# Performance work log

Hardware: AMD Instinct MI355X
Metric: run time of the kernel (lower is better)

## Reference

```python
import jax, jax.numpy as jnp
import numpy as np

B, D = 8192, 256
NUM_CLASSES = 128
CHUNK = 256          # matches module chunk_size; B % CHUNK == 0
TEMP = 0.07
EPS_NORM = 1e-12


def setup_inputs() -> dict:
    key = jax.random.key(0)
    k1, k2 = jax.random.split(key)
    features = jax.random.normal(k1, (B, D), dtype=jnp.float32)
    labels = jax.random.randint(k2, (B,), 0, NUM_CLASSES, dtype=jnp.int64)
    return {"features": features, "labels": labels}


def reference(features, labels):
    n = features.shape[0]
    temperature = max(TEMP, 1e-4)

    # F.normalize(dim=1): x / max(||x||, eps)
    norm = jnp.maximum(jnp.linalg.norm(features, axis=1, keepdims=True), EPS_NORM)
    f = features / norm
    # clamp is a no-op after normalization but kept for faithfulness
    f = jnp.clip(f, -1000.0, 1000.0)

    # [B, B] similarity; the torch loop computes exactly these rows chunk by chunk
    sim = jnp.matmul(f, f.T) / temperature

    # self-mask: each row i masks column i (diagonal of its chunk's square block)
    self_mask = ~jnp.eye(n, dtype=bool)

    # positive mask: same label, excluding self
    pos = (labels[:, None] == labels[None, :]) & self_mask
    # per-chunk fallback: if a 256-row chunk has no positives at all, use self_mask
    pos_c = pos.reshape(n // CHUNK, CHUNK, n)
    has_pos = pos_c.any(axis=(1, 2), keepdims=True)
    pos = jnp.where(has_pos, pos_c, self_mask.reshape(n // CHUNK, CHUNK, n)).reshape(n, n)

    # max-subtract BEFORE self-masking (faithful: includes self-sim = 1/temp)
    sim_max = jnp.max(sim, axis=1, keepdims=True)
    logits = jnp.clip(sim - jax.lax.stop_gradient(sim_max), -1000.0, 1000.0)

    exp_sim = jnp.maximum(jnp.exp(logits), 1e-8) * self_mask
    log_sum_exp = jnp.log(jnp.sum(exp_sim, axis=1, keepdims=True) + 1e-8)
    log_prob = jnp.maximum(logits - log_sum_exp, -1000.0)

    pos_pairs = jnp.sum(pos, axis=1)                      # [B] int
    row_loss = -jnp.sum(pos * log_prob, axis=1)           # [B]
    valid = pos_pairs > 0
    row_loss = jnp.where(valid, row_loss / jnp.maximum(pos_pairs, 1).astype(row_loss.dtype), 0.0)

    total_loss = jnp.sum(row_loss)
    total_pairs = jnp.sum(valid).astype(jnp.float32)
    mean_loss = total_loss / (total_pairs + 1e-8)
    loss = mean_loss  # reduction == 'mean'
    return loss, total_pairs, mean_loss
```

## Files before the change

### kernel.cpp

```cpp
#include <hip/hip_runtime.h>
#include <hip/hip_bf16.h>
#include <type_traits>

#define NB 8192
#define DD 256
#define INV_T (1.0f/0.07f)
#define LOG2E 1.4426950408889634f
#define LN2   0.6931471805599453f
#define K1    (INV_T*LOG2E)
#define NSPLIT 8
#define BM 128
#define BN 64
#define CPS (NB/NSPLIT)
#define NITER (CPS/BN)
#define BUFB (BN*DD*2)

typedef __attribute__((ext_vector_type(8))) short s8v;
typedef __attribute__((ext_vector_type(4))) float f4v;
typedef unsigned int u32;
typedef unsigned short u16;

#define OFF_FB   0
#define OFF_SE   (4*1024*1024)
#define OFF_SP   (OFF_SE + NSPLIT*NB*4)
#define OFF_CL   (OFF_SP + NSPLIT*NB*4)
#define OFF_CV   (OFF_CL + 256)
#define OFF_CNT  (OFF_CV + 256)

__global__ void k_norm(const float* __restrict__ feat,
                       __hip_bfloat16* __restrict__ fb, int* __restrict__ cnt) {
    if (blockIdx.x == 0 && threadIdx.x == 0) *cnt = 0;
    const int t = threadIdx.x;
    const int w = t >> 6, l = t & 63;
    const int row = blockIdx.x * 4 + w;
    const float4 v = ((const float4*)feat)[row * 64 + l];
    float s = v.x * v.x + v.y * v.y + v.z * v.z + v.w * v.w;
    #pragma unroll
    for (int d = 32; d; d >>= 1) s += __shfl_xor(s, d, 64);
    const float scale = 1.0f / fmaxf(sqrtf(s), 1e-12f);
    __hip_bfloat16 h0 = __float2bfloat16(v.x * scale);
    __hip_bfloat16 h1 = __float2bfloat16(v.y * scale);
    __hip_bfloat16 h2 = __float2bfloat16(v.z * scale);
    __hip_bfloat16 h3 = __float2bfloat16(v.w * scale);
    ushort4 o;
    o.x = *(u16*)&h0; o.y = *(u16*)&h1; o.z = *(u16*)&h2; o.w = *(u16*)&h3;
    ((ushort4*)fb)[row * 64 + l] = o;
}

__launch_bounds__(256, 2)
__global__ void k_main(const __hip_bfloat16* __restrict__ fb,
                       const int* __restrict__ lab,
                       float* __restrict__ SE, float* __restrict__ SP) {
    __shared__ __align__(16) char ldsB[2 * BUFB];
    __shared__ int ldsLab[CPS];
    const int tid = threadIdx.x;
    const int l = tid & 63;
    const int l15 = l & 15, lg = l >> 4;
    const int bid = blockIdx.x;
    const int sp = bid & 7, rb = bid >> 3;
    const int wbase = rb * BM + (tid >> 6) * 32;
    const int col0 = sp * CPS;

    #pragma unroll
    for (int i = 0; i < 4; i++)
        ldsLab[tid + i * 256] = lab[col0 + tid + i * 256];

    s8v a[2][8];
    #pragma unroll
    for (int m = 0; m < 2; m++)
        #pragma unroll
        for (int kk = 0; kk < 8; kk++)
            a[m][kk] = *(const s8v*)(fb + (wbase + m * 16 + l15) * DD + kk * 32 + lg * 8);

    int labr[8];
    #pragma unroll
    for (int m = 0; m < 2; m++)
        #pragma unroll
        for (int r = 0; r < 4; r++)
            labr[m * 4 + r] = lab[wbase + m * 16 + lg * 4 + r];

    float sE[8], sPp[8];
    #pragma unroll
    for (int i = 0; i < 8; i++) { sE[i] = 0.f; sPp[i] = 0.f; }

    s8v st[8];
    auto load_tile = [&](int t) {
        const char* gsrc = (const char*)fb + (size_t)(col0 + t * BN) * (DD * 2);
        #pragma unroll
        for (int i = 0; i < 8; i++)
            st[i] = *(const s8v*)(gsrc + tid * 16 + i * 4096);
    };
    auto write_tile = [&](int bufoff) {
        #pragma unroll
        for (int i = 0; i < 8; i++) {
            const int x = tid * 16 + i * 4096;
            const int br = x >> 9, inrow = x & 511;
            *(s8v*)(ldsB + bufoff + (br * 512 | (inrow ^ ((br & 7) << 4)))) = st[i];
        }
    };

    auto run = [&](auto diagC) {
        constexpr bool DIAG = decltype(diagC)::value;
        load_tile(0);
        write_tile(0);
        __syncthreads();
        for (int t = 0; t < NITER; t++) {
            const int curoff = (t & 1) * BUFB;
            if (t + 1 < NITER) load_tile(t + 1);

            f4v acc[2][4];
            #pragma unroll
            for (int m = 0; m < 2; m++)
                #pragma unroll
                for (int n = 0; n < 4; n++)
                    acc[m][n] = (f4v){0.f, 0.f, 0.f, 0.f};

            #pragma unroll
            for (int kk = 0; kk < 8; kk++) {
                s8v bfr[4];
                #pragma unroll
                for (int n = 0; n < 4; n++) {
                    const int br = n * 16 + l15;
                    const int ad = (br * 512 + kk * 64 + lg * 16) ^ ((br & 7) << 4);
                    bfr[n] = *(const s8v*)(ldsB + curoff + ad);
                }
                #pragma unroll
                for (int m = 0; m < 2; m++)
                    #pragma unroll
                    for (int n = 0; n < 4; n++)
                        acc[m][n] = __builtin_amdgcn_mfma_f32_16x16x32_bf16(a[m][kk], bfr[n], acc[m][n], 0, 0, 0);
            }

            const int cb = col0 + t * BN;
            #pragma unroll
            for (int n = 0; n < 4; n++) {
                const int col = cb + n * 16 + l15;
                const int lc = ldsLab[t * BN + n * 16 + l15];
                #pragma unroll
                for (int m = 0; m < 2; m++)
                    #pragma unroll
                    for (int r = 0; r < 4; r++) {
                        const int idx = m * 4 + r;
                        const float lg2 = fmaf(acc[m][n][r], K1, -K1);
                        float e = fmaxf(exp2f(lg2), 1e-8f);
                        bool pos = (lc == labr[idx]);
                        if (DIAG) {
                            const int row = wbase + m * 16 + lg * 4 + r;
                            const bool nself = (row != col);
                            e = nself ? e : 0.f;
                            pos = pos && nself;
                        }
                        sE[idx] += e;
                        sPp[idx] += pos ? lg2 : 0.f;
                    }
            }

            if (t + 1 < NITER) write_tile(curoff ^ BUFB);
            __syncthreads();
        }
    };
    if ((rb >> 3) == sp) run(std::true_type{}); else run(std::false_type{});

    #pragma unroll
    for (int idx = 0; idx < 8; idx++) {
        #pragma unroll
        for (int d = 1; d < 16; d <<= 1) {
            sE[idx]  += __shfl_xor(sE[idx], d, 16);
            sPp[idx] += __shfl_xor(sPp[idx], d, 16);
        }
    }
    if (l15 == 0) {
        #pragma unroll
        for (int idx = 0; idx < 8; idx++) {
            const int row = wbase + (idx >> 2) * 16 + lg * 4 + (idx & 3);
            SE[sp * NB + row] = sE[idx];
            SP[sp * NB + row] = sPp[idx];
        }
    }
}

__global__ void k_rows(const int* __restrict__ lab,
                       const float* __restrict__ SE, const float* __restrict__ SP,
                       float* __restrict__ CL, float* __restrict__ CV,
                       int* __restrict__ cnt, float* __restrict__ out) {
    __shared__ int h[128];
    const int t = threadIdx.x;
    if (t < 128) h[t] = 0;
    __syncthreads();
    #pragma unroll
    for (int i = 0; i < 32; i++)
        atomicAdd(&h[lab[t + i * 256]], 1);
    __syncthreads();

    const int row = blockIdx.x * 256 + t;
    float se = 0.f, sp_ = 0.f;
    #pragma unroll
    for (int s = 0; s < NSPLIT; s++) {
        se  += SE[s * NB + row];
        sp_ += SP[s * NB + row];
    }
    const int n = h[lab[row]] - 1;
    const float lse = logf(se + 1e-8f);
    const bool valid = n > 0;
    float loss = valid ? (lse - sp_ * LN2 / (float)n) : 0.f;
    float vf = valid ? 1.f : 0.f;
    #pragma unroll
    for (int d = 32; d; d >>= 1) { loss += __shfl_xor(loss, d, 64); vf += __shfl_xor(vf, d, 64); }
    __shared__ float pl[4], pv[4];
    __shared__ int isLast;
    if ((t & 63) == 0) { pl[t >> 6] = loss; pv[t >> 6] = vf; }
    __syncthreads();
    if (t == 0) {
        CL[blockIdx.x] = pl[0] + pl[1] + pl[2] + pl[3];
        CV[blockIdx.x] = pv[0] + pv[1] + pv[2] + pv[3];
        __threadfence();
        isLast = (atomicAdd(cnt, 1) == 31);
    }
    __syncthreads();
    if (isLast) {
        __threadfence();
        float lsum = (t < 32) ? CL[t] : 0.f;
        float vsum = (t < 32) ? CV[t] : 0.f;
        #pragma unroll
        for (int d = 32; d; d >>= 1) { lsum += __shfl_xor(lsum, d, 64); vsum += __shfl_xor(vsum, d, 64); }
        if (t == 0) {
            const float mean = lsum / (vsum + 1e-8f);
            out[0] = mean;
            out[1] = vsum;
            out[2] = mean;
        }
    }
}

extern "C" void kernel_launch(void* const* d_in, const int* in_sizes, int n_in,
                              void* d_out, int out_size, void* d_ws, size_t ws_size,
                              hipStream_t stream) {
    (void)in_sizes; (void)n_in; (void)out_size; (void)ws_size;
    const float* feat = (const float*)d_in[0];
    const int*   lab  = (const int*)d_in[1];
    char* ws = (char*)d_ws;
    __hip_bfloat16* fb = (__hip_bfloat16*)(ws + OFF_FB);
    float* SE = (float*)(ws + OFF_SE);
    float* SP = (float*)(ws + OFF_SP);
    float* CL = (float*)(ws + OFF_CL);
    float* CV = (float*)(ws + OFF_CV);
    int*   cnt = (int*)(ws + OFF_CNT);
    float* out = (float*)d_out;

    hipLaunchKernelGGL(k_norm, dim3(NB / 4), dim3(256), 0, stream, feat, fb, cnt);
    hipLaunchKernelGGL(k_main, dim3(NB / BM * NSPLIT), dim3(256), 0, stream, fb, lab, SE, SP);
    hipLaunchKernelGGL(k_rows, dim3(NB / 256), dim3(256), 0, stream, lab, SE, SP, CL, CV, cnt, out);
}
```

Baseline: 71.67 us.

## Use 512-thread blocks and fold temperature offset into the final reduction

Row-block size doubles to 256 with 512-thread workgroups, so each LDS column tile is shared by 8 waves and each thread loads half as much of it. The epilogue drops the per-element fma and the 1e-8 clamp: it exponentiates sim*K1 directly and sums raw dot products for positives. The constant max offset (exp(-1/T) and n/T) is applied once per row in k_rows. Dropping the clamp slightly changes semantics for tiny exponentials, and the larger block may reduce occupancy and block-level scheduling flexibility.

```diff
diff --git a/kernel.cpp b/kernel.cpp
--- a/kernel.cpp
+++ b/kernel.cpp
@@ -6,10 +6,10 @@
 #define DD 256
 #define INV_T (1.0f/0.07f)
 #define LOG2E 1.4426950408889634f
-#define LN2   0.6931471805599453f
 #define K1    (INV_T*LOG2E)
+#define CEXP  6.2087204553847255e-7f
 #define NSPLIT 8
-#define BM 128
+#define BM 256
 #define BN 64
 #define CPS (NB/NSPLIT)
 #define NITER (CPS/BN)
@@ -47,7 +47,7 @@
     ((ushort4*)fb)[row * 64 + l] = o;
 }
 
-__launch_bounds__(256, 2)
+__launch_bounds__(512)
 __global__ void k_main(const __hip_bfloat16* __restrict__ fb,
                        const int* __restrict__ lab,
                        float* __restrict__ SE, float* __restrict__ SP) {
@@ -61,9 +61,8 @@
     const int wbase = rb * BM + (tid >> 6) * 32;
     const int col0 = sp * CPS;
 
-    #pragma unroll
-    for (int i = 0; i < 4; i++)
-        ldsLab[tid + i * 256] = lab[col0 + tid + i * 256];
+    ldsLab[tid]       = lab[col0 + tid];
+    ldsLab[tid + 512] = lab[col0 + 512 + tid];
 
     s8v a[2][8];
     #pragma unroll
@@ -79,21 +78,21 @@
         for (int r = 0; r < 4; r++)
             labr[m * 4 + r] = lab[wbase + m * 16 + lg * 4 + r];
 
-    float sE[8], sPp[8];
-    #pragma unroll
-    for (int i = 0; i < 8; i++) { sE[i] = 0.f; sPp[i] = 0.f; }
-
-    s8v st[8];
+    float sE[8], sPa[8];
+    #pragma unroll
+    for (int i = 0; i < 8; i++) { sE[i] = 0.f; sPa[i] = 0.f; }
+
+    s8v st[4];
     auto load_tile = [&](int t) {
         const char* gsrc = (const char*)fb + (size_t)(col0 + t * BN) * (DD * 2);
         #pragma unroll
-        for (int i = 0; i < 8; i++)
-            st[i] = *(const s8v*)(gsrc + tid * 16 + i * 4096);
+        for (int i = 0; i < 4; i++)
+            st[i] = *(const s8v*)(gsrc + tid * 16 + i * 8192);
     };
     auto write_tile = [&](int bufoff) {
         #pragma unroll
-        for (int i = 0; i < 8; i++) {
-            const int x = tid * 16 + i * 4096;
+        for (int i = 0; i < 4; i++) {
+            const int x = tid * 16 + i * 8192;
             const int br = x >> 9, inrow = x & 511;
             *(s8v*)(ldsB + bufoff + (br * 512 | (inrow ^ ((br & 7) << 4)))) = st[i];
         }
@@ -108,6 +107,11 @@
             const int curoff = (t & 1) * BUFB;
             if (t + 1 < NITER) load_tile(t + 1);
 
+            int lc[4];
+            #pragma unroll
+            for (int n = 0; n < 4; n++)
+                lc[n] = ldsLab[t * BN + n * 16 + l15];
+
             f4v acc[2][4];
             #pragma unroll
             for (int m = 0; m < 2; m++)
@@ -117,56 +121,67 @@
 
             #pragma unroll
             for (int kk = 0; kk < 8; kk++) {
-                s8v bfr[4];
-                #pragma unroll
-                for (int n = 0; n < 4; n++) {
-                    const int br = n * 16 + l15;
-                    const int ad = (br * 512 + kk * 64 + lg * 16) ^ ((br & 7) << 4);
-                    bfr[n] = *(const s8v*)(ldsB + curoff + ad);
+                s8v b0, b1;
+                {
+                    const int br0 = 0 * 16 + l15, br1 = 1 * 16 + l15;
+                    b0 = *(const s8v*)(ldsB + curoff + ((br0 * 512 + kk * 64 + lg * 16) ^ ((br0 & 7) << 4)));
+                    b1 = *(const s8v*)(ldsB + curoff + ((br1 * 512 + kk * 64 + lg * 16) ^ ((br1 & 7) << 4)));
                 }
-                #pragma unroll
-                for (int m = 0; m < 2; m++)
-                    #pragma unroll
-                    for (int n = 0; n < 4; n++)
-                        acc[m][n] = __builtin_amdgcn_mfma_f32_16x16x32_bf16(a[m][kk], bfr[n], acc[m][n], 0, 0, 0);
+                acc[0][0] = __builtin_amdgcn_mfma_f32_16x16x32_bf16(a[0][kk], b0, acc[0][0], 0, 0, 0);
+                acc[1][0] = __builtin_amdgcn_mfma_f32_16x16x32_bf16(a[1][kk], b0, acc[1][0], 0, 0, 0);
+                acc[0][1] = __builtin_amdgcn_mfma_f32_16x16x32_bf16(a[0][kk], b1, acc[0][1], 0, 0, 0);
+                acc[1][1] = __builtin_amdgcn_mfma_f32_16x16x32_bf16(a[1][kk], b1, acc[1][1], 0, 0, 0);
             }
+            #pragma unroll
+            for (int kk = 0; kk < 8; kk++) {
+                s8v b2, b3;
+                {
+                    const int br2 = 2 * 16 + l15, br3 = 3 * 16 + l15;
+                    b2 = *(const s8v*)(ldsB + curoff + ((br2 * 512 + kk * 64 + lg * 16) ^ ((br2 & 7) << 4)));
+                    b3 = *(const s8v*)(ldsB + curoff + ((br3 * 512 + kk * 64 + lg * 16) ^ ((br3 & 7) << 4)));
+                }
+                acc[0][2] = __builtin_amdgcn_mfma_f32_16x16x32_bf16(a[0][kk], b2, acc[0][2], 0, 0, 0);
+                acc[1][2] = __builtin_amdgcn_mfma_f32_16x16x32_bf16(a[1][kk], b2, acc[1][2], 0, 0, 0);
+                acc[0][3] = __builtin_amdgcn_mfma_f32_16x16x32_bf16(a[0][kk], b3, acc[0][3], 0, 0, 0);
+                acc[1][3] = __builtin_amdgcn_mfma_f32_16x16x32_bf16(a[1][kk], b3, acc[1][3], 0, 0, 0);
+            }
 
             const int cb = col0 + t * BN;
-            #pragma unroll
-            for (int n = 0; n < 4; n++) {
-                const int col = cb + n * 16 + l15;
-                const int lc = ldsLab[t * BN + n * 16 + l15];
+            auto ep = [&](int n) {
                 #pragma unroll
                 for (int m = 0; m < 2; m++)
                     #pragma unroll
                     for (int r = 0; r < 4; r++) {
                         const int idx = m * 4 + r;
-                        const float lg2 = fmaf(acc[m][n][r], K1, -K1);
-                        float e = fmaxf(exp2f(lg2), 1e-8f);
-                        bool pos = (lc == labr[idx]);
+                        const float v = acc[m][n][r];
+                        float e = exp2f(v * K1);
+                        bool pos = (lc[n] == labr[idx]);
                         if (DIAG) {
                             const int row = wbase + m * 16 + lg * 4 + r;
+                            const int col = cb + n * 16 + l15;
                             const bool nself = (row != col);
                             e = nself ? e : 0.f;
                             pos = pos && nself;
                         }
                         sE[idx] += e;
-                        sPp[idx] += pos ? lg2 : 0.f;
+                        sPa[idx] += pos ? v : 0.f;
                     }
-            }
+            };
+            ep(0); ep(1);
+            ep(2); ep(3);
 
             if (t + 1 < NITER) write_tile(curoff ^ BUFB);
             __syncthreads();
         }
     };
-    if ((rb >> 3) == sp) run(std::true_type{}); else run(std::false_type{});
+    if ((rb >> 2) == sp) run(std::true_type{}); else run(std::false_type{});
 
     #pragma unroll
     for (int idx = 0; idx < 8; idx++) {
         #pragma unroll
         for (int d = 1; d < 16; d <<= 1) {
             sE[idx]  += __shfl_xor(sE[idx], d, 16);
-            sPp[idx] += __shfl_xor(sPp[idx], d, 16);
+            sPa[idx] += __shfl_xor(sPa[idx], d, 16);
         }
     }
     if (l15 == 0) {
@@ -174,7 +189,7 @@
         for (int idx = 0; idx < 8; idx++) {
             const int row = wbase + (idx >> 2) * 16 + lg * 4 + (idx & 3);
             SE[sp * NB + row] = sE[idx];
-            SP[sp * NB + row] = sPp[idx];
+            SP[sp * NB + row] = sPa[idx];
         }
     }
 }
@@ -193,16 +208,16 @@
     __syncthreads();
 
     const int row = blockIdx.x * 256 + t;
-    float se = 0.f, sp_ = 0.f;
+    float se = 0.f, spa = 0.f;
     #pragma unroll
     for (int s = 0; s < NSPLIT; s++) {
         se  += SE[s * NB + row];
-        sp_ += SP[s * NB + row];
+        spa += SP[s * NB + row];
     }
     const int n = h[lab[row]] - 1;
-    const float lse = logf(se + 1e-8f);
+    const float lse = logf(se * CEXP + 1e-8f);
     const bool valid = n > 0;
-    float loss = valid ? (lse - sp_ * LN2 / (float)n) : 0.f;
+    float loss = valid ? (lse - (spa - (float)n) * INV_T / (float)n) : 0.f;
     float vf = valid ? 1.f : 0.f;
     #pragma unroll
     for (int d = 32; d; d >>= 1) { loss += __shfl_xor(loss, d, 64); vf += __shfl_xor(vf, d, 64); }
@@ -248,6 +263,6 @@
     float* out = (float*)d_out;
 
     hipLaunchKernelGGL(k_norm, dim3(NB / 4), dim3(256), 0, stream, feat, fb, cnt);
-    hipLaunchKernelGGL(k_main, dim3(NB / BM * NSPLIT), dim3(256), 0, stream, fb, lab, SE, SP);
+    hipLaunchKernelGGL(k_main, dim3(NB / BM * NSPLIT), dim3(512), 0, stream, fb, lab, SE, SP);
     hipLaunchKernelGGL(k_rows, dim3(NB / 256), dim3(256), 0, stream, lab, SE, SP, CL, CV, cnt, out);
 }
```

Result: no change. 70.73 us (-1.3%).

## Exploit similarity symmetry: compute upper-triangle tiles and emit row and column partial sums

Applied to the files above, without the earlier changes.

The main kernel now iterates only over upper-triangular 256x256 tiles (528 blocks of 512 threads), using the symmetry of f·fᵀ. Each off-diagonal tile accumulates both row sums and column sums, the column sums via shuffles and LDS, so the MFMA work is roughly halved. The max-subtraction is also moved out of the inner loop: exp2(v*K1) is accumulated unshifted and rescaled by a constant in the row kernel, and the positive sum is now stored as raw similarity. This adds column-reduction overhead and 32-way partial arrays that the final kernel must read. It also relies on unshifted exponentials staying in range, which holds because the features are normalized.

```diff
diff --git a/kernel.cpp b/kernel.cpp
--- a/kernel.cpp
+++ b/kernel.cpp
@@ -6,13 +6,12 @@
 #define DD 256
 #define INV_T (1.0f/0.07f)
 #define LOG2E 1.4426950408889634f
-#define LN2   0.6931471805599453f
 #define K1    (INV_T*LOG2E)
-#define NSPLIT 8
-#define BM 128
+#define CEXP  6.2087204553847255e-7f
+#define NSTRIP 32
+#define TILE 256
 #define BN 64
-#define CPS (NB/NSPLIT)
-#define NITER (CPS/BN)
+#define NITER 4
 #define BUFB (BN*DD*2)
 
 typedef __attribute__((ext_vector_type(8))) short s8v;
@@ -22,8 +21,8 @@
 
 #define OFF_FB   0
 #define OFF_SE   (4*1024*1024)
-#define OFF_SP   (OFF_SE + NSPLIT*NB*4)
-#define OFF_CL   (OFF_SP + NSPLIT*NB*4)
+#define OFF_SP   (OFF_SE + NSTRIP*NB*4)
+#define OFF_CL   (OFF_SP + NSTRIP*NB*4)
 #define OFF_CV   (OFF_CL + 256)
 #define OFF_CNT  (OFF_CV + 256)
 
@@ -47,23 +46,26 @@
     ((ushort4*)fb)[row * 64 + l] = o;
 }
 
-__launch_bounds__(256, 2)
+__launch_bounds__(512)
 __global__ void k_main(const __hip_bfloat16* __restrict__ fb,
                        const int* __restrict__ lab,
                        float* __restrict__ SE, float* __restrict__ SP) {
     __shared__ __align__(16) char ldsB[2 * BUFB];
-    __shared__ int ldsLab[CPS];
+    __shared__ int ldsLab[TILE];
+    __shared__ float ldsColE[8][TILE];
+    __shared__ float ldsColP[8][TILE];
     const int tid = threadIdx.x;
+    const int w = tid >> 6;
     const int l = tid & 63;
     const int l15 = l & 15, lg = l >> 4;
-    const int bid = blockIdx.x;
-    const int sp = bid & 7, rb = bid >> 3;
-    const int wbase = rb * BM + (tid >> 6) * 32;
-    const int col0 = sp * CPS;
-
-    #pragma unroll
-    for (int i = 0; i < 4; i++)
-        ldsLab[tid + i * 256] = lab[col0 + tid + i * 256];
+
+    int cb = 0, rem = blockIdx.x;
+    while (rem >= NSTRIP - cb) { rem -= NSTRIP - cb; cb++; }
+    const int rb = cb + rem;
+    const int row0 = rb * TILE, col0 = cb * TILE;
+    const int wbase = row0 + w * 32;
+
+    if (tid < TILE) ldsLab[tid] = lab[col0 + tid];
 
     s8v a[2][8];
     #pragma unroll
@@ -79,21 +81,23 @@
         for (int r = 0; r < 4; r++)
             labr[m * 4 + r] = lab[wbase + m * 16 + lg * 4 + r];
 
-    float sE[8], sPp[8];
-    #pragma unroll
-    for (int i = 0; i < 8; i++) { sE[i] = 0.f; sPp[i] = 0.f; }
-
-    s8v st[8];
-    auto load_tile = [&](int t) {
-        const char* gsrc = (const char*)fb + (size_t)(col0 + t * BN) * (DD * 2);
-        #pragma unroll
-        for (int i = 0; i < 8; i++)
-            st[i] = *(const s8v*)(gsrc + tid * 16 + i * 4096);
+    float sE[8], sPa[8], colE[4], colP[4];
+    #pragma unroll
+    for (int i = 0; i < 8; i++) { sE[i] = 0.f; sPa[i] = 0.f; }
+    #pragma unroll
+    for (int i = 0; i < 4; i++) { colE[i] = 0.f; colP[i] = 0.f; }
+
+    s8v st[4];
+    auto load_tile = [&](int ct) {
+        const char* gsrc = (const char*)fb + (size_t)(col0 + ct * BN) * (DD * 2);
+        #pragma unroll
+        for (int i = 0; i < 4; i++)
+            st[i] = *(const s8v*)(gsrc + tid * 16 + i * 8192);
     };
     auto write_tile = [&](int bufoff) {
         #pragma unroll
-        for (int i = 0; i < 8; i++) {
-            const int x = tid * 16 + i * 4096;
+        for (int i = 0; i < 4; i++) {
+            const int x = tid * 16 + i * 8192;
             const int br = x >> 9, inrow = x & 511;
             *(s8v*)(ldsB + bufoff + (br * 512 | (inrow ^ ((br & 7) << 4)))) = st[i];
         }
@@ -104,9 +108,14 @@
         load_tile(0);
         write_tile(0);
         __syncthreads();
-        for (int t = 0; t < NITER; t++) {
-            const int curoff = (t & 1) * BUFB;
-            if (t + 1 < NITER) load_tile(t + 1);
+        for (int ct = 0; ct < NITER; ct++) {
+            const int curoff = (ct & 1) * BUFB;
+            if (ct + 1 < NITER) load_tile(ct + 1);
+
+            int lc[4];
+            #pragma unroll
+            for (int n = 0; n < 4; n++)
+                lc[n] = ldsLab[ct * BN + n * 16 + l15];
 
             f4v acc[2][4];
             #pragma unroll
@@ -131,50 +140,85 @@
                         acc[m][n] = __builtin_amdgcn_mfma_f32_16x16x32_bf16(a[m][kk], bfr[n], acc[m][n], 0, 0, 0);
             }
 
-            const int cb = col0 + t * BN;
             #pragma unroll
             for (int n = 0; n < 4; n++) {
-                const int col = cb + n * 16 + l15;
-                const int lc = ldsLab[t * BN + n * 16 + l15];
                 #pragma unroll
                 for (int m = 0; m < 2; m++)
                     #pragma unroll
                     for (int r = 0; r < 4; r++) {
                         const int idx = m * 4 + r;
-                        const float lg2 = fmaf(acc[m][n][r], K1, -K1);
-                        float e = fmaxf(exp2f(lg2), 1e-8f);
-                        bool pos = (lc == labr[idx]);
+                        const float v = acc[m][n][r];
+                        float e = exp2f(v * K1);
+                        bool pos = (lc[n] == labr[idx]);
                         if (DIAG) {
                             const int row = wbase + m * 16 + lg * 4 + r;
-                            const bool nself = (row != col);
+                            const int coln = col0 + ct * BN + n * 16 + l15;
+                            const bool nself = (row != coln);
                             e = nself ? e : 0.f;
                             pos = pos && nself;
                         }
+                        const float pv = pos ? v : 0.f;
                         sE[idx] += e;
-                        sPp[idx] += pos ? lg2 : 0.f;
+                        sPa[idx] += pv;
+                        if (!DIAG) { colE[n] += e; colP[n] += pv; }
                     }
             }
 
-            if (t + 1 < NITER) write_tile(curoff ^ BUFB);
+            if (!DIAG) {
+                #pragma unroll
+                for (int n = 0; n < 4; n++) {
+                    colE[n] += __shfl_xor(colE[n], 16, 64);
+                    colE[n] += __shfl_xor(colE[n], 32, 64);
+                    colP[n] += __shfl_xor(colP[n], 16, 64);
+                    colP[n] += __shfl_xor(colP[n], 32, 64);
+                }
+                if (l < 16) {
+                    #pragma unroll
+                    for (int n = 0; n < 4; n++) {
+                        ldsColE[w][ct * BN + n * 16 + l15] = colE[n];
+                        ldsColP[w][ct * BN + n * 16 + l15] = colP[n];
+                    }
+                }
+                #pragma unroll
+                for (int n = 0; n < 4; n++) { colE[n] = 0.f; colP[n] = 0.f; }
+            }
+
+            if (ct + 1 < NITER) write_tile(curoff ^ BUFB);
             __syncthreads();
         }
     };
-    if ((rb >> 3) == sp) run(std::true_type{}); else run(std::false_type{});
+    if (rb == cb) run(std::true_type{}); else run(std::false_type{});
 
     #pragma unroll
     for (int idx = 0; idx < 8; idx++) {
         #pragma unroll
         for (int d = 1; d < 16; d <<= 1) {
             sE[idx]  += __shfl_xor(sE[idx], d, 16);
-            sPp[idx] += __shfl_xor(sPp[idx], d, 16);
+            sPa[idx] += __shfl_xor(sPa[idx], d, 16);
         }
     }
     if (l15 == 0) {
         #pragma unroll
         for (int idx = 0; idx < 8; idx++) {
             const int row = wbase + (idx >> 2) * 16 + lg * 4 + (idx & 3);
-            SE[sp * NB + row] = sE[idx];
-            SP[sp * NB + row] = sPp[idx];
+            SE[cb * NB + row] = sE[idx];
+            SP[cb * NB + row] = sPa[idx];
+        }
+    }
+
+    if (rb != cb) {
+        __syncthreads();
+        const int c = tid & 255;
+        if (tid < 256) {
+            float s = 0.f;
+            #pragma unroll
+            for (int w2 = 0; w2 < 8; w2++) s += ldsColE[w2][c];
+            SE[rb * NB + col0 + c] = s;
+        } else {
+            float s = 0.f;
+            #pragma unroll
+            for (int w2 = 0; w2 < 8; w2++) s += ldsColP[w2][c];
+            SP[rb * NB + col0 + c] = s;
         }
     }
 }
@@ -193,16 +237,16 @@
     __syncthreads();
 
     const int row = blockIdx.x * 256 + t;
-    float se = 0.f, sp_ = 0.f;
-    #pragma unroll
-    for (int s = 0; s < NSPLIT; s++) {
+    float se = 0.f, spa = 0.f;
+    #pragma unroll
+    for (int s = 0; s < NSTRIP; s++) {
         se  += SE[s * NB + row];
-        sp_ += SP[s * NB + row];
+        spa += SP[s * NB + row];
     }
     const int n = h[lab[row]] - 1;
-    const float lse = logf(se + 1e-8f);
+    const float lse = logf(se * CEXP + 1e-8f);
     const bool valid = n > 0;
-    float loss = valid ? (lse - sp_ * LN2 / (float)n) : 0.f;
+    float loss = valid ? (lse - (spa - (float)n) * INV_T / (float)n) : 0.f;
     float vf = valid ? 1.f : 0.f;
     #pragma unroll
     for (int d = 32; d; d >>= 1) { loss += __shfl_xor(loss, d, 64); vf += __shfl_xor(vf, d, 64); }
@@ -248,6 +292,6 @@
     float* out = (float*)d_out;
 
     hipLaunchKernelGGL(k_norm, dim3(NB / 4), dim3(256), 0, stream, feat, fb, cnt);
-    hipLaunchKernelGGL(k_main, dim3(NB / BM * NSPLIT), dim3(256), 0, stream, fb, lab, SE, SP);
+    hipLaunchKernelGGL(k_main, dim3(528), dim3(512), 0, stream, fb, lab, SE, SP);
     hipLaunchKernelGGL(k_rows, dim3(NB / 256), dim3(256), 0, stream, lab, SE, SP, CL, CV, cnt, out);
 }
```

Result: slower. 74.22 us (+3.6%).
